# Kernel tuning notes

Measured on AMD Instinct MI355X. Metric: run time of the kernel, lower is better.

## Reference

```python
import jax, jax.numpy as jnp
import numpy as np

N_NODES = 100000
N_EDGES = 3200000
D_IN = 128
D_OUT = 128


def setup_inputs() -> dict:
    key = jax.random.key(0)
    k1, k2, k3, k4 = jax.random.split(key, 4)
    x = jax.random.normal(k1, (N_NODES, D_IN), dtype=jnp.float32)
    W = jax.random.normal(k2, (D_OUT, D_IN), dtype=jnp.float32) * (1.0 / np.sqrt(D_IN))
    edge_weight = jax.random.uniform(k3, (N_EDGES,), dtype=jnp.float32)
    edge_index = jax.random.randint(k4, (2, N_EDGES), 0, N_NODES, dtype=jnp.int32)
    return {"x": x, "W": W, "edge_weight": edge_weight, "edge_index": edge_index}


def reference(x, W, edge_weight, edge_index):
    # spmm(flt, x): for each edge (r, c, w): agg[r] += w * x[c]
    rows = edge_index[0]
    cols = edge_index[1]
    msgs = edge_weight[:, None] * x[cols]                      # [E, D_IN]
    agg = jax.ops.segment_sum(msgs, rows, num_segments=x.shape[0])  # [N, D_IN]
    # nn.Linear(bias=False): agg @ W.T, then tanh activation
    return jnp.tanh(agg @ W.T)
```

## Files before the change

### kernel.cpp

```cpp
#include <hip/hip_runtime.h>
#include <hip/hip_fp16.h>
#include <cstdint>

#define NN 100000
#define NE 3200000
#define DD 128

#define NB 782
#define NBP 800
#define T3 6400
#define EPT 25

#define CAP 5120
#define RPT 20

typedef __attribute__((ext_vector_type(8))) short s8v;
typedef __attribute__((ext_vector_type(4))) float f4v;

__device__ __forceinline__ unsigned f2bf(float f) {
    unsigned u = __float_as_uint(f);
    return (u + 0x7fffu + ((u >> 16) & 1u)) >> 16;
}
__device__ __forceinline__ float bf2f(unsigned b) { return __uint_as_float(b << 16); }
__device__ __forceinline__ unsigned packhl(float v) {
    unsigned h = f2bf(v);
    unsigned l = f2bf(v - bf2f(h));
    return (h << 16) | l;
}
__device__ __forceinline__ float tanh_fast(float x) {
    float e = __expf(2.0f * x);
    return 1.0f - 2.0f / (e + 1.0f);
}

__global__ __launch_bounds__(256) void xcvt_k(
    const float* __restrict__ x, __half* __restrict__ xh)
{
    int i = (blockIdx.x * 256 + threadIdx.x) * 4;
    float4 v = *reinterpret_cast<const float4*>(x + i);
    __half2 a = __floats2half2_rn(v.x, v.y);
    __half2 b = __floats2half2_rn(v.z, v.w);
    uint2 o = { *reinterpret_cast<unsigned*>(&a), *reinterpret_cast<unsigned*>(&b) };
    *reinterpret_cast<uint2*>(xh + i) = o;
}

__global__ __launch_bounds__(256) void tile_scatter_k(
    const int* __restrict__ rows, const int* __restrict__ cols,
    const float* __restrict__ ew, int* __restrict__ bin_cursor,
    unsigned* __restrict__ b4, unsigned char* __restrict__ nloc)
{
    __shared__ int h[NBP];
    __shared__ int toff[NBP];
    __shared__ int pos[NBP];
    __shared__ int gb[NBP];
    __shared__ int ps[256];
    __shared__ unsigned rec4[T3];
    __shared__ unsigned char nl[T3];

    int t = threadIdx.x;
    int base = blockIdx.x * T3;

    for (int b = t; b < NBP; b += 256) h[b] = 0;
    __syncthreads();

    int rv[EPT];
    #pragma unroll
    for (int i = 0; i < EPT; ++i) {
        int e = base + i * 256 + t;
        rv[i] = rows[e];
        atomicAdd(&h[rv[i] >> 7], 1);
    }
    __syncthreads();

    int c[4]; int s0 = 0;
    #pragma unroll
    for (int j = 0; j < 4; ++j) {
        int b = 4 * t + j;
        c[j] = (b < NBP) ? h[b] : 0;
        s0 += c[j];
    }
    ps[t] = s0; __syncthreads();
    for (int off = 1; off < 256; off <<= 1) {
        int add = (t >= off) ? ps[t - off] : 0;
        __syncthreads();
        ps[t] += add;
        __syncthreads();
    }
    int excl = ps[t] - s0;
    #pragma unroll
    for (int j = 0; j < 4; ++j) {
        int b = 4 * t + j;
        if (b < NBP) { toff[b] = excl; pos[b] = excl; excl += c[j]; }
    }
    __syncthreads();

    for (int b = t; b < NB; b += 256)
        gb[b] = h[b] ? atomicAdd(&bin_cursor[b], h[b]) : 0;
    __syncthreads();

    #pragma unroll
    for (int i = 0; i < EPT; ++i) {
        int e = base + i * 256 + t;
        int r = rv[i];
        int b = r >> 7;
        int slot = atomicAdd(&pos[b], 1);
        float w = ew[e];
        int wfx = (int)(w * 32768.0f + 0.5f);
        if (wfx > 32767) wfx = 32767;
        rec4[slot] = (unsigned)cols[e] | ((unsigned)wfx << 17);
        nl[slot]   = (unsigned char)(r & 127);
    }
    __syncthreads();

    {
        int idx = EPT * t;
        int end_i = idx + EPT;
        int lo = 0, hi = NB - 1;
        while (lo < hi) {
            int mid = (lo + hi + 1) >> 1;
            if (toff[mid] <= idx) lo = mid; else hi = mid - 1;
        }
        int b2 = lo;
        for (; idx < end_i; ++idx) {
            while (idx >= toff[b2] + h[b2]) ++b2;
            int rel = gb[b2] + (idx - toff[b2]);
            if (rel < CAP) {
                size_t d = (size_t)b2 * CAP + rel;
                b4[d]   = rec4[idx];
                nloc[d] = nl[idx];
            }
        }
    }
}

__global__ __launch_bounds__(256) void sort_bin_k(
    const int* __restrict__ bin_cursor,
    unsigned* __restrict__ b4, const unsigned char* __restrict__ nloc,
    int* __restrict__ node_off, int* __restrict__ node_cnt)
{
    __shared__ unsigned rec[CAP];
    __shared__ int lh[128], sc[128], lpos[128];

    int b = blockIdx.x, t = threadIdx.x;
    size_t start = (size_t)b * CAP;
    int cnt = bin_cursor[b];
    if (cnt > CAP) cnt = CAP;

    unsigned mr[RPT]; int mn[RPT];
    #pragma unroll
    for (int j = 0; j < RPT; ++j) {
        int idx = t + j * 256;
        mr[j] = (idx < cnt) ? b4[start + idx] : 0u;
        mn[j] = (idx < cnt) ? (int)nloc[start + idx] : 0;
    }

    if (t < 128) lh[t] = 0;
    __syncthreads();
    #pragma unroll
    for (int j = 0; j < RPT; ++j) {
        int idx = t + j * 256;
        if (idx < cnt) atomicAdd(&lh[mn[j]], 1);
    }
    __syncthreads();

    int v = (t < 128) ? lh[t] : 0;
    if (t < 128) sc[t] = v;
    __syncthreads();
    for (int off = 1; off < 128; off <<= 1) {
        int add = (t >= off && t < 128) ? sc[t - off] : 0;
        __syncthreads();
        if (t < 128) sc[t] += add;
        __syncthreads();
    }
    if (t < 128) {
        int excl = sc[t] - v;
        lpos[t] = excl;
        int node = b * 128 + t;
        if (node < NN) {
            node_off[node] = (int)start + excl;
            node_cnt[node] = v;
        }
    }
    __syncthreads();

    #pragma unroll
    for (int j = 0; j < RPT; ++j) {
        int idx = t + j * 256;
        if (idx < cnt) {
            int slot = atomicAdd(&lpos[mn[j]], 1);
            rec[slot] = mr[j];
        }
    }
    __syncthreads();

    for (int i = t; i < cnt; i += 256)
        b4[start + i] = rec[i];
}

__global__ __launch_bounds__(256) void gather_hf_k(
    const unsigned* __restrict__ xh,
    const unsigned* __restrict__ b4,
    const int* __restrict__ node_off, const int* __restrict__ node_cnt,
    unsigned* __restrict__ aggp)
{
    int node = blockIdx.x * 4 + (threadIdx.x >> 6);
    int lane = threadIdx.x & 63;
    int start = node_off[node];
    int end   = start + node_cnt[node];

    float2 acc = {0.f, 0.f};
    int i = start;
    for (; i + 7 < end; i += 8) {
        unsigned e[8]; unsigned v[8];
        #pragma unroll
        for (int j = 0; j < 8; ++j) e[j] = b4[i + j];
        #pragma unroll
        for (int j = 0; j < 8; ++j)
            v[j] = xh[(size_t)(e[j] & 0x1FFFFu) * 64 + lane];
        #pragma unroll
        for (int j = 0; j < 8; ++j) {
            float w = (float)(e[j] >> 17) * (1.0f / 32768.0f);
            __half2 h2 = *reinterpret_cast<__half2*>(&v[j]);
            float2 f2 = __half22float2(h2);
            acc.x += w * f2.x;
            acc.y += w * f2.y;
        }
    }
    for (; i < end; ++i) {
        unsigned e0 = b4[i];
        unsigned v0 = xh[(size_t)(e0 & 0x1FFFFu) * 64 + lane];
        float w = (float)(e0 >> 17) * (1.0f / 32768.0f);
        __half2 h2 = *reinterpret_cast<__half2*>(&v0);
        float2 f2 = __half22float2(h2);
        acc.x += w * f2.x;
        acc.y += w * f2.y;
    }

    uint2 o;
    o.x = packhl(acc.x);
    o.y = packhl(acc.y);
    reinterpret_cast<uint2*>(aggp + (size_t)node * DD)[lane] = o;
}

__device__ __forceinline__ int wswz(int o, int k) {
    int byte = (o << 8) + (k << 1);
    byte ^= (o & 7) << 4;
    return byte >> 1;
}
__device__ __forceinline__ void unpack8(uint4 a, uint4 b, s8v& hi, s8v& lo) {
    unsigned u[8] = {a.x, a.y, a.z, a.w, b.x, b.y, b.z, b.w};
    #pragma unroll
    for (int j = 0; j < 8; ++j) {
        hi[j] = (short)(u[j] >> 16);
        lo[j] = (short)(u[j] & 0xffffu);
    }
}

__global__ __launch_bounds__(256) void gemm_mfma_k(
    const unsigned* __restrict__ aggp, const float* __restrict__ W,
    float* __restrict__ out)
{
    __shared__ __align__(16) unsigned short Wh[128 * 128];
    __shared__ __align__(16) unsigned short Wl[128 * 128];

    int t = threadIdx.x;
    for (int i = t; i < 128 * 128; i += 256) {
        int o = i >> 7, k = i & 127;
        float f = W[i];
        unsigned h = f2bf(f);
        unsigned l = f2bf(f - bf2f(h));
        int idx = wswz(o, k);
        Wh[idx] = (unsigned short)h;
        Wl[idx] = (unsigned short)l;
    }
    __syncthreads();

    int lane = t & 63;
    int w    = t >> 6;
    int rbase = blockIdx.x * 128 + w * 32;
    int fr = lane & 15, fq = lane >> 4;

    f4v acc[2][8];
    #pragma unroll
    for (int rt = 0; rt < 2; ++rt)
        #pragma unroll
        for (int nt = 0; nt < 8; ++nt)
            acc[rt][nt] = 0.0f;

    #pragma unroll
    for (int ks = 0; ks < 4; ++ks) {
        int kb = ks * 32 + fq * 8;
        s8v ah[2], al[2];
        #pragma unroll
        for (int rt = 0; rt < 2; ++rt) {
            int r = rbase + rt * 16 + fr;
            int rc = (r < NN) ? r : (NN - 1);
            const uint4* p = reinterpret_cast<const uint4*>(aggp + (size_t)rc * DD + kb);
            unpack8(p[0], p[1], ah[rt], al[rt]);
        }
        #pragma unroll
        for (int nt = 0; nt < 8; ++nt) {
            int o = nt * 16 + fr;
            int kk = ks * 32 + fq * 8;
            s8v bh = *reinterpret_cast<const s8v*>(&Wh[wswz(o, kk)]);
            s8v bl = *reinterpret_cast<const s8v*>(&Wl[wswz(o, kk)]);
            #pragma unroll
            for (int rt = 0; rt < 2; ++rt) {
                acc[rt][nt] = __builtin_amdgcn_mfma_f32_16x16x32_bf16(ah[rt], bh, acc[rt][nt], 0, 0, 0);
                acc[rt][nt] = __builtin_amdgcn_mfma_f32_16x16x32_bf16(al[rt], bh, acc[rt][nt], 0, 0, 0);
                acc[rt][nt] = __builtin_amdgcn_mfma_f32_16x16x32_bf16(ah[rt], bl, acc[rt][nt], 0, 0, 0);
            }
        }
    }

    #pragma unroll
    for (int rt = 0; rt < 2; ++rt) {
        int rr = rbase + rt * 16 + fq * 4;
        #pragma unroll
        for (int nt = 0; nt < 8; ++nt) {
            int col = nt * 16 + fr;
            #pragma unroll
            for (int j = 0; j < 4; ++j) {
                int row = rr + j;
                if (row < NN)
                    out[(size_t)row * DD + col] = tanh_fast(acc[rt][nt][j]);
            }
        }
    }
}

__global__ __launch_bounds__(256) void scatter_k(
    const float* __restrict__ x, const float* __restrict__ ew,
    const int* __restrict__ rows, const int* __restrict__ cols,
    float* __restrict__ agg)
{
    int e    = blockIdx.x * 4 + (threadIdx.x >> 6);
    int lane = threadIdx.x & 63;
    int r = rows[e];
    int c = cols[e];
    float w = ew[e];
    float2 v = reinterpret_cast<const float2*>(x + (size_t)c * DD)[lane];
    float* ag = agg + (size_t)r * DD + lane * 2;
    atomicAdd(ag,     w * v.x);
    atomicAdd(ag + 1, w * v.y);
}

__global__ __launch_bounds__(256) void gemm_tanh_k(
    const float* __restrict__ agg, const float* __restrict__ W,
    float* __restrict__ out)
{
    __shared__ float Wt[DD][DD + 4];
    __shared__ float At[32][DD];

    int tid = threadIdx.x;
    for (int i = tid; i < DD * DD; i += 256) {
        int o = i >> 7, k = i & 127;
        Wt[k][o] = W[i];
    }
    int row0 = blockIdx.x * 32;
    for (int i = tid; i < 32 * DD; i += 256) {
        At[i >> 7][i & 127] = agg[(size_t)row0 * DD + i];
    }
    __syncthreads();

    int colg = tid & 31;
    int rowg = tid >> 5;
    int c0 = colg * 4;
    int r0 = rowg * 4;

    float acc[4][4] = {};
    for (int k = 0; k < DD; ++k) {
        float4 wv = *reinterpret_cast<const float4*>(&Wt[k][c0]);
        #pragma unroll
        for (int i = 0; i < 4; ++i) {
            float a = At[r0 + i][k];
            acc[i][0] += a * wv.x;
            acc[i][1] += a * wv.y;
            acc[i][2] += a * wv.z;
            acc[i][3] += a * wv.w;
        }
    }

    #pragma unroll
    for (int i = 0; i < 4; ++i) {
        int r = row0 + r0 + i;
        float4 o4 = { tanhf(acc[i][0]), tanhf(acc[i][1]),
                      tanhf(acc[i][2]), tanhf(acc[i][3]) };
        *reinterpret_cast<float4*>(&out[(size_t)r * DD + c0]) = o4;
    }
}

extern "C" void kernel_launch(void* const* d_in, const int* in_sizes, int n_in,
                              void* d_out, int out_size, void* d_ws, size_t ws_size,
                              hipStream_t stream) {
    const float* x  = (const float*)d_in[0];
    const float* W  = (const float*)d_in[1];
    const float* ew = (const float*)d_in[2];
    const int*   ei = (const int*)d_in[3];
    const int* rows = ei;
    const int* cols = ei + NE;
    float* out = (float*)d_out;
    unsigned* aggp = (unsigned*)d_out;

    size_t ints = (size_t)NB + (size_t)2 * NN;
    size_t hdr = (ints + 3) & ~(size_t)3;
    size_t nbucket = (size_t)NB * CAP;
    size_t need = hdr * 4 + nbucket * 4 + (size_t)NN * 64 * 4 + nbucket;

    if (ws_size >= need) {
        int* bin_cursor = (int*)d_ws;
        int* node_off   = bin_cursor + NB;
        int* node_cnt   = node_off + NN;
        unsigned* b4    = (unsigned*)((int*)d_ws + hdr);
        unsigned* xh    = b4 + nbucket;
        unsigned char* nloc = (unsigned char*)(xh + (size_t)NN * 64);

        hipMemsetAsync(bin_cursor, 0, (size_t)NB * sizeof(int), stream);
        xcvt_k<<<NN * DD / 1024, 256, 0, stream>>>(x, (__half*)xh);
        tile_scatter_k<<<NE / T3, 256, 0, stream>>>(rows, cols, ew, bin_cursor, b4, nloc);
        sort_bin_k<<<NB, 256, 0, stream>>>(bin_cursor, b4, nloc, node_off, node_cnt);
        gather_hf_k<<<NN / 4, 256, 0, stream>>>(xh, b4, node_off, node_cnt, aggp);
        gemm_mfma_k<<<NB, 256, 0, stream>>>(aggp, W, out);
    } else {
        hipMemsetAsync(out, 0, (size_t)NN * DD * sizeof(float), stream);
        scatter_k<<<NE / 4, 256, 0, stream>>>(x, ew, rows, cols, out);
        gemm_tanh_k<<<NN / 32, 256, 0, stream>>>(out, W, out);
    }
}
```

Before: 287.5 us.

## Precompute split-bf16 W once, coalesce bin scatter writes, nontemporal edge loads

```diff
diff --git a/kernel.cpp b/kernel.cpp
--- a/kernel.cpp
+++ b/kernel.cpp
@@ -30,6 +30,11 @@
 __device__ __forceinline__ float tanh_fast(float x) {
     float e = __expf(2.0f * x);
     return 1.0f - 2.0f / (e + 1.0f);
+}
+__device__ __forceinline__ int wswz(int o, int k) {
+    int byte = (o << 8) + (k << 1);
+    byte ^= (o & 7) << 4;
+    return byte >> 1;
 }
 
 __global__ __launch_bounds__(256) void xcvt_k(
@@ -41,6 +46,19 @@
     __half2 b = __floats2half2_rn(v.z, v.w);
     uint2 o = { *reinterpret_cast<unsigned*>(&a), *reinterpret_cast<unsigned*>(&b) };
     *reinterpret_cast<uint2*>(xh + i) = o;
+}
+
+__global__ __launch_bounds__(256) void wcvt_k(
+    const float* __restrict__ W, unsigned short* __restrict__ whl)
+{
+    int i = blockIdx.x * 256 + threadIdx.x;
+    int o = i >> 7, k = i & 127;
+    float f = W[i];
+    unsigned h = f2bf(f);
+    unsigned l = f2bf(f - bf2f(h));
+    int idx = wswz(o, k);
+    whl[idx]         = (unsigned short)h;
+    whl[16384 + idx] = (unsigned short)l;
 }
 
 __global__ __launch_bounds__(256) void tile_scatter_k(
@@ -111,23 +129,19 @@
     }
     __syncthreads();
 
-    {
-        int idx = EPT * t;
-        int end_i = idx + EPT;
+    int wid = t >> 6, lane = t & 63;
+    for (int chunk = wid; chunk < T3 / 64; chunk += 4) {
+        int idx = chunk * 64 + lane;
         int lo = 0, hi = NB - 1;
         while (lo < hi) {
             int mid = (lo + hi + 1) >> 1;
             if (toff[mid] <= idx) lo = mid; else hi = mid - 1;
         }
-        int b2 = lo;
-        for (; idx < end_i; ++idx) {
-            while (idx >= toff[b2] + h[b2]) ++b2;
-            int rel = gb[b2] + (idx - toff[b2]);
-            if (rel < CAP) {
-                size_t d = (size_t)b2 * CAP + rel;
-                b4[d]   = rec4[idx];
-                nloc[d] = nl[idx];
-            }
+        int rel = gb[lo] + (idx - toff[lo]);
+        if (rel < CAP) {
+            size_t d = (size_t)lo * CAP + rel;
+            b4[d]   = rec4[idx];
+            nloc[d] = nl[idx];
         }
     }
 }
@@ -212,7 +226,7 @@
     for (; i + 7 < end; i += 8) {
         unsigned e[8]; unsigned v[8];
         #pragma unroll
-        for (int j = 0; j < 8; ++j) e[j] = b4[i + j];
+        for (int j = 0; j < 8; ++j) e[j] = __builtin_nontemporal_load(b4 + i + j);
         #pragma unroll
         for (int j = 0; j < 8; ++j)
             v[j] = xh[(size_t)(e[j] & 0x1FFFFu) * 64 + lane];
@@ -241,11 +255,6 @@
     reinterpret_cast<uint2*>(aggp + (size_t)node * DD)[lane] = o;
 }
 
-__device__ __forceinline__ int wswz(int o, int k) {
-    int byte = (o << 8) + (k << 1);
-    byte ^= (o & 7) << 4;
-    return byte >> 1;
-}
 __device__ __forceinline__ void unpack8(uint4 a, uint4 b, s8v& hi, s8v& lo) {
     unsigned u[8] = {a.x, a.y, a.z, a.w, b.x, b.y, b.z, b.w};
     #pragma unroll
@@ -256,21 +265,22 @@
 }
 
 __global__ __launch_bounds__(256) void gemm_mfma_k(
-    const unsigned* __restrict__ aggp, const float* __restrict__ W,
+    const unsigned* __restrict__ aggp, const unsigned short* __restrict__ whl,
     float* __restrict__ out)
 {
     __shared__ __align__(16) unsigned short Wh[128 * 128];
     __shared__ __align__(16) unsigned short Wl[128 * 128];
 
     int t = threadIdx.x;
-    for (int i = t; i < 128 * 128; i += 256) {
-        int o = i >> 7, k = i & 127;
-        float f = W[i];
-        unsigned h = f2bf(f);
-        unsigned l = f2bf(f - bf2f(h));
-        int idx = wswz(o, k);
-        Wh[idx] = (unsigned short)h;
-        Wl[idx] = (unsigned short)l;
+    {
+        const uint4* src = reinterpret_cast<const uint4*>(whl);
+        uint4* dh = reinterpret_cast<uint4*>(Wh);
+        uint4* dl = reinterpret_cast<uint4*>(Wl);
+        #pragma unroll
+        for (int i = 0; i < 8; ++i) {
+            dh[t + i * 256] = src[t + i * 256];
+            dl[t + i * 256] = src[2048 + t + i * 256];
+        }
     }
     __syncthreads();
 
@@ -404,7 +414,7 @@
     size_t ints = (size_t)NB + (size_t)2 * NN;
     size_t hdr = (ints + 3) & ~(size_t)3;
     size_t nbucket = (size_t)NB * CAP;
-    size_t need = hdr * 4 + nbucket * 4 + (size_t)NN * 64 * 4 + nbucket;
+    size_t need = hdr * 4 + nbucket * 4 + (size_t)NN * 64 * 4 + nbucket + 65536;
 
     if (ws_size >= need) {
         int* bin_cursor = (int*)d_ws;
@@ -413,13 +423,15 @@
         unsigned* b4    = (unsigned*)((int*)d_ws + hdr);
         unsigned* xh    = b4 + nbucket;
         unsigned char* nloc = (unsigned char*)(xh + (size_t)NN * 64);
+        unsigned short* whl = (unsigned short*)(nloc + nbucket);
 
         hipMemsetAsync(bin_cursor, 0, (size_t)NB * sizeof(int), stream);
         xcvt_k<<<NN * DD / 1024, 256, 0, stream>>>(x, (__half*)xh);
+        wcvt_k<<<64, 256, 0, stream>>>(W, whl);
         tile_scatter_k<<<NE / T3, 256, 0, stream>>>(rows, cols, ew, bin_cursor, b4, nloc);
         sort_bin_k<<<NB, 256, 0, stream>>>(bin_cursor, b4, nloc, node_off, node_cnt);
         gather_hf_k<<<NN / 4, 256, 0, stream>>>(xh, b4, node_off, node_cnt, aggp);
-        gemm_mfma_k<<<NB, 256, 0, stream>>>(aggp, W, out);
+        gemm_mfma_k<<<NB, 256, 0, stream>>>(aggp, whl, out);
     } else {
         hipMemsetAsync(out, 0, (size_t)NN * DD * sizeof(float), stream);
         scatter_k<<<NE / 4, 256, 0, stream>>>(x, ew, rows, cols, out);
```

New measurement: 267.0 us. 1.08x faster.
